# Kernel tuning notes

Hardware: AMD Instinct MI355X
Metric: run time of the kernel (lower is better)

The kernel has to match this reference:

```python
import jax, jax.numpy as jnp
import numpy as np
import math

INPUT_DIM = 1024
OUTPUT_DIM = 8192
M_BLOCKS = 8  # ceil(OUTPUT_DIM / INPUT_DIM)
SCALE = 1.0


def fwht(x):
    """Unnormalized fast Walsh-Hadamard transform over the last axis.
    Matches the torch recursive-cat implementation (Sylvester/natural order).
    """
    n = x.shape[-1]
    lead = x.shape[:-1]
    h = 1
    while h < n:
        y = x.reshape(lead + (n // (2 * h), 2, h))
        a = y[..., 0, :]
        b = y[..., 1, :]
        x = jnp.stack([a + b, a - b], axis=-2).reshape(lead + (n,))
        h *= 2
    return x


def setup_inputs() -> dict:
    key = jax.random.key(0)
    kx, kb, kg, ks, kp, ku = jax.random.split(key, 6)
    x = jax.random.normal(kx, (8, 1024, INPUT_DIM), dtype=jnp.float32)
    B = jax.random.normal(kb, (M_BLOCKS, INPUT_DIM), dtype=jnp.float32)
    G = jax.random.normal(kg, (M_BLOCKS, INPUT_DIM), dtype=jnp.float32)
    S = jax.random.uniform(ks, (M_BLOCKS, INPUT_DIM), dtype=jnp.float32)
    P = jax.random.randint(kp, (M_BLOCKS, INPUT_DIM), 0, INPUT_DIM, dtype=jnp.int64)
    u_rand = jax.random.uniform(ku, (OUTPUT_DIM,), dtype=jnp.float32)
    return {"x": x, "B": B, "G": G, "S": S, "P": P, "u_rand": u_rand}


def reference(x, B, G, S, P, u_rand):
    d = INPUT_DIM
    # flatten all leading dims into rows: (R, 1, d)
    xr = x.reshape(-1, 1, d)
    Bx = xr * B                                   # (R, m, d)
    HBx = fwht(Bx)                                # (R, m, d)
    idx = jnp.broadcast_to(P[None], HBx.shape)    # per-block permutation gather
    PHBx = jnp.take_along_axis(HBx, idx, axis=-1)
    GPHBx = PHBx * G
    HGPHBx = fwht(GPHBx)
    SHGPHBx = HGPHBx * S
    norm_factor = 1.0 / (SCALE * math.sqrt(d))
    Vx = norm_factor * SHGPHBx.reshape(SHGPHBx.shape[0], -1)  # (R, m*d)
    result = Vx[:, :OUTPUT_DIM]
    # phi nonlinearity: cos(x + 2*pi*U) * sqrt(2/output_dim)
    phase = (2.0 * jnp.pi) * u_rand
    result = jnp.cos(result + phase) * math.sqrt(2.0 / OUTPUT_DIM)
    return result
```

## Files before the change

### kernel.cpp

```cpp
#include <hip/hip_runtime.h>
#include <math.h>


typedef unsigned uint2_ev __attribute__((ext_vector_type(2)));
typedef float    f32x4    __attribute__((ext_vector_type(4)));

template <int CTRL>
__device__ __forceinline__ float dpp_f(float x) {
    return __int_as_float(
        __builtin_amdgcn_mov_dpp(__float_as_int(x), CTRL, 0xF, 0xF, true));
}

#define DPP_XOR1 0xB1
#define DPP_XOR2 0x4E
#define DPP_XOR3 0x1B
#define DPP_HMIR 0x141
#define DPP_ROR8 0x128

__device__ __forceinline__ void pl16_pair(float& e0, float& e1) {
    uint2_ev r = __builtin_amdgcn_permlane16_swap(
        __float_as_uint(e0), __float_as_uint(e1), false, false);
    float s = __uint_as_float(r.x) + __uint_as_float(r.y);
    float d = __uint_as_float(r.x) - __uint_as_float(r.y);
    uint2_ev q = __builtin_amdgcn_permlane16_swap(
        __float_as_uint(s), __float_as_uint(d), false, false);
    e0 = __uint_as_float(q.x);
    e1 = __uint_as_float(q.y);
}

__device__ __forceinline__ void pl32_pair(float& e0, float& e1) {
    uint2_ev r = __builtin_amdgcn_permlane32_swap(
        __float_as_uint(e0), __float_as_uint(e1), false, false);
    float s = __uint_as_float(r.x) + __uint_as_float(r.y);
    float d = __uint_as_float(r.x) - __uint_as_float(r.y);
    uint2_ev q = __builtin_amdgcn_permlane32_swap(
        __float_as_uint(s), __float_as_uint(d), false, false);
    e0 = __uint_as_float(q.x);
    e1 = __uint_as_float(q.y);
}

__device__ __forceinline__ void fwht_full(float v[16], float sg0, float sg1,
                                          float sg2, float sg3) {
#pragma unroll
    for (int h = 1; h < 16; h <<= 1) {
#pragma unroll
        for (int k = 0; k < 16; ++k) {
            if (!(k & h)) {
                float a = v[k], b = v[k ^ h];
                v[k] = a + b;
                v[k ^ h] = a - b;
            }
        }
    }
#pragma unroll
    for (int k = 0; k < 16; ++k) v[k] = fmaf(v[k], sg0, dpp_f<DPP_XOR1>(v[k]));
#pragma unroll
    for (int k = 0; k < 16; ++k) v[k] = fmaf(v[k], sg1, dpp_f<DPP_XOR2>(v[k]));
#pragma unroll
    for (int k = 0; k < 16; ++k)
        v[k] = fmaf(v[k], sg2, dpp_f<DPP_XOR3>(dpp_f<DPP_HMIR>(v[k])));
#pragma unroll
    for (int k = 0; k < 16; ++k) v[k] = fmaf(v[k], sg3, dpp_f<DPP_ROR8>(v[k]));
#pragma unroll
    for (int p = 0; p < 8; ++p) pl16_pair(v[2 * p], v[2 * p + 1]);
#pragma unroll
    for (int p = 0; p < 8; ++p) pl32_pair(v[2 * p], v[2 * p + 1]);
}

__global__ __launch_bounds__(256) void fastfood_kernel(
    const float* __restrict__ x, const float* __restrict__ B,
    const float* __restrict__ G, const float* __restrict__ S,
    const int* __restrict__ P, const float* __restrict__ u_rand,
    float* __restrict__ out)
{
    __shared__ float lds[4 * 1088];
    const int lane = threadIdx.x & 63;
    const int wv   = threadIdx.x >> 6;
    const int gw   = blockIdx.x * 4 + wv;
    const int row  = gw >> 3;
    const int mo   = (gw & 7) << 10;

    const float sg0 = (lane & 1) ? -1.f : 1.f;
    const float sg1 = (lane & 2) ? -1.f : 1.f;
    const float sg2 = (lane & 4) ? -1.f : 1.f;
    const float sg3 = (lane & 8) ? -1.f : 1.f;

    float* wlds = lds + wv * 1088;
    float4* w4 = (float4*)(wlds + 16 * lane + 4 * (lane >> 2));

    const float c_arg = 0.03125f * 0.15915494309189535f;
    const float c_amp = 0.015625f;

    float v[16];

    {
        const float4* x4 = (const float4*)(x + (size_t)row * 1024 + 16 * lane);
        const float4* B4 = (const float4*)(B + mo + 16 * lane);
#pragma unroll
        for (int j = 0; j < 4; ++j) {
            float4 xt = x4[j];
            float4 bt = B4[j];
            v[4 * j + 0] = xt.x * bt.x;
            v[4 * j + 1] = xt.y * bt.y;
            v[4 * j + 2] = xt.z * bt.z;
            v[4 * j + 3] = xt.w * bt.w;
        }
    }

    fwht_full(v, sg0, sg1, sg2, sg3);

    const int4*   P4 = (const int4*)(P + mo);
    const float4* G4 = (const float4*)(G + mo);
    int4   pj[4];
    float4 gj[4];
#pragma unroll
    for (int j = 0; j < 4; ++j) {
        pj[j] = P4[64 * j + lane];
        gj[j] = G4[64 * j + lane];
    }

#pragma unroll
    for (int j = 0; j < 4; ++j)
        w4[j] = make_float4(v[4 * j + 0], v[4 * j + 1],
                            v[4 * j + 2], v[4 * j + 3]);

#pragma unroll
    for (int j = 0; j < 4; ++j) {
        int4 p = pj[j];
        float4 g = gj[j];
        v[4 * j + 0] = wlds[p.x + ((p.x >> 6) << 2)] * g.x;
        v[4 * j + 1] = wlds[p.y + ((p.y >> 6) << 2)] * g.y;
        v[4 * j + 2] = wlds[p.z + ((p.z >> 6) << 2)] * g.z;
        v[4 * j + 3] = wlds[p.w + ((p.w >> 6) << 2)] * g.w;
    }

    float4 sv[4], uv[4];
    {
        const float4* S4 = (const float4*)(S + mo);
        const float4* U4 = (const float4*)(u_rand + mo);
#pragma unroll
        for (int b = 0; b < 4; ++b) {
            int idx = b * 64 + lane;
            sv[b] = S4[idx];
            uv[b] = U4[idx];
        }
    }

    fwht_full(v, sg0, sg1, sg2, sg3);

    {
        f32x4* o4 = (f32x4*)(out + (size_t)row * 8192 + mo);
#pragma unroll
        for (int b = 0; b < 4; ++b) {
            int idx = b * 64 + lane;
            f32x4 rr;
            rr.x = __builtin_amdgcn_cosf(__builtin_amdgcn_fractf(
                       fmaf(v[4 * b + 0] * sv[b].x, c_arg, uv[b].x))) * c_amp;
            rr.y = __builtin_amdgcn_cosf(__builtin_amdgcn_fractf(
                       fmaf(v[4 * b + 1] * sv[b].y, c_arg, uv[b].y))) * c_amp;
            rr.z = __builtin_amdgcn_cosf(__builtin_amdgcn_fractf(
                       fmaf(v[4 * b + 2] * sv[b].z, c_arg, uv[b].z))) * c_amp;
            rr.w = __builtin_amdgcn_cosf(__builtin_amdgcn_fractf(
                       fmaf(v[4 * b + 3] * sv[b].w, c_arg, uv[b].w))) * c_amp;
            __builtin_nontemporal_store(rr, &o4[idx]);
        }
    }
}

extern "C" void kernel_launch(void* const* d_in, const int* in_sizes, int n_in,
                              void* d_out, int out_size, void* d_ws, size_t ws_size,
                              hipStream_t stream) {
    const float* x = (const float*)d_in[0];
    const float* B = (const float*)d_in[1];
    const float* G = (const float*)d_in[2];
    const float* S = (const float*)d_in[3];
    const int*   P = (const int*)d_in[4];
    const float* u = (const float*)d_in[5];
    float* out = (float*)d_out;

    dim3 grid(16384), block(256);
    hipLaunchKernelGGL(fastfood_kernel, grid, block, 0, stream,
                       x, B, G, S, P, u, out);
}
```

Before: 342.1 us.

## Process all eight blocks per wave with loop, reusing x row in registers

Each wave now handles one full row and loops over the eight output blocks instead of one wave per (row, block). The x row is loaded once with nontemporal loads and kept in registers, and the next block's B vector is prefetched a block ahead. Output stores become regular stores instead of nontemporal. The grid shrinks eightfold, which cuts x reloads but reduces parallelism and serializes per-wave work.

```diff
diff --git a/kernel.cpp b/kernel.cpp
--- a/kernel.cpp
+++ b/kernel.cpp
@@ -76,9 +76,7 @@
     __shared__ float lds[4 * 1088];
     const int lane = threadIdx.x & 63;
     const int wv   = threadIdx.x >> 6;
-    const int gw   = blockIdx.x * 4 + wv;
-    const int row  = gw >> 3;
-    const int mo   = (gw & 7) << 10;
+    const int row  = blockIdx.x * 4 + wv;
 
     const float sg0 = (lane & 1) ? -1.f : 1.f;
     const float sg1 = (lane & 2) ? -1.f : 1.f;
@@ -91,78 +89,103 @@
     const float c_arg = 0.03125f * 0.15915494309189535f;
     const float c_amp = 0.015625f;
 
-    float v[16];
-
+    float xv[16];
     {
-        const float4* x4 = (const float4*)(x + (size_t)row * 1024 + 16 * lane);
-        const float4* B4 = (const float4*)(B + mo + 16 * lane);
+        const f32x4* x4 = (const f32x4*)(x + (size_t)row * 1024 + 16 * lane);
 #pragma unroll
         for (int j = 0; j < 4; ++j) {
-            float4 xt = x4[j];
-            float4 bt = B4[j];
-            v[4 * j + 0] = xt.x * bt.x;
-            v[4 * j + 1] = xt.y * bt.y;
-            v[4 * j + 2] = xt.z * bt.z;
-            v[4 * j + 3] = xt.w * bt.w;
-        }
-    }
-
-    fwht_full(v, sg0, sg1, sg2, sg3);
-
-    const int4*   P4 = (const int4*)(P + mo);
-    const float4* G4 = (const float4*)(G + mo);
-    int4   pj[4];
-    float4 gj[4];
-#pragma unroll
-    for (int j = 0; j < 4; ++j) {
-        pj[j] = P4[64 * j + lane];
-        gj[j] = G4[64 * j + lane];
-    }
-
-#pragma unroll
-    for (int j = 0; j < 4; ++j)
-        w4[j] = make_float4(v[4 * j + 0], v[4 * j + 1],
-                            v[4 * j + 2], v[4 * j + 3]);
-
-#pragma unroll
-    for (int j = 0; j < 4; ++j) {
-        int4 p = pj[j];
-        float4 g = gj[j];
-        v[4 * j + 0] = wlds[p.x + ((p.x >> 6) << 2)] * g.x;
-        v[4 * j + 1] = wlds[p.y + ((p.y >> 6) << 2)] * g.y;
-        v[4 * j + 2] = wlds[p.z + ((p.z >> 6) << 2)] * g.z;
-        v[4 * j + 3] = wlds[p.w + ((p.w >> 6) << 2)] * g.w;
-    }
-
-    float4 sv[4], uv[4];
+            f32x4 t = __builtin_nontemporal_load(&x4[j]);
+            xv[4 * j + 0] = t.x; xv[4 * j + 1] = t.y;
+            xv[4 * j + 2] = t.z; xv[4 * j + 3] = t.w;
+        }
+    }
+
+    float4 Bn0, Bn1, Bn2, Bn3;
     {
-        const float4* S4 = (const float4*)(S + mo);
-        const float4* U4 = (const float4*)(u_rand + mo);
-#pragma unroll
-        for (int b = 0; b < 4; ++b) {
-            int idx = b * 64 + lane;
-            sv[b] = S4[idx];
-            uv[b] = U4[idx];
-        }
-    }
-
-    fwht_full(v, sg0, sg1, sg2, sg3);
-
-    {
-        f32x4* o4 = (f32x4*)(out + (size_t)row * 8192 + mo);
-#pragma unroll
-        for (int b = 0; b < 4; ++b) {
-            int idx = b * 64 + lane;
-            f32x4 rr;
-            rr.x = __builtin_amdgcn_cosf(__builtin_amdgcn_fractf(
-                       fmaf(v[4 * b + 0] * sv[b].x, c_arg, uv[b].x))) * c_amp;
-            rr.y = __builtin_amdgcn_cosf(__builtin_amdgcn_fractf(
-                       fmaf(v[4 * b + 1] * sv[b].y, c_arg, uv[b].y))) * c_amp;
-            rr.z = __builtin_amdgcn_cosf(__builtin_amdgcn_fractf(
-                       fmaf(v[4 * b + 2] * sv[b].z, c_arg, uv[b].z))) * c_amp;
-            rr.w = __builtin_amdgcn_cosf(__builtin_amdgcn_fractf(
-                       fmaf(v[4 * b + 3] * sv[b].w, c_arg, uv[b].w))) * c_amp;
-            __builtin_nontemporal_store(rr, &o4[idx]);
+        const float4* B4 = (const float4*)(B + 16 * lane);
+        Bn0 = B4[0]; Bn1 = B4[1]; Bn2 = B4[2]; Bn3 = B4[3];
+    }
+
+#pragma unroll 1
+    for (int m = 0; m < 8; ++m) {
+        const int mo = m << 10;
+
+        float4 Bc0 = Bn0, Bc1 = Bn1, Bc2 = Bn2, Bc3 = Bn3;
+        {
+            const float4* Bq =
+                (const float4*)(B + (m < 7 ? mo + 1024 : mo) + 16 * lane);
+            Bn0 = Bq[0]; Bn1 = Bq[1]; Bn2 = Bq[2]; Bn3 = Bq[3];
+        }
+
+        float v[16];
+        v[0]  = xv[0]  * Bc0.x; v[1]  = xv[1]  * Bc0.y;
+        v[2]  = xv[2]  * Bc0.z; v[3]  = xv[3]  * Bc0.w;
+        v[4]  = xv[4]  * Bc1.x; v[5]  = xv[5]  * Bc1.y;
+        v[6]  = xv[6]  * Bc1.z; v[7]  = xv[7]  * Bc1.w;
+        v[8]  = xv[8]  * Bc2.x; v[9]  = xv[9]  * Bc2.y;
+        v[10] = xv[10] * Bc2.z; v[11] = xv[11] * Bc2.w;
+        v[12] = xv[12] * Bc3.x; v[13] = xv[13] * Bc3.y;
+        v[14] = xv[14] * Bc3.z; v[15] = xv[15] * Bc3.w;
+
+        int4   pj[4];
+        float4 gj[4];
+        {
+            const int4*   P4 = (const int4*)(P + mo);
+            const float4* G4 = (const float4*)(G + mo);
+#pragma unroll
+            for (int j = 0; j < 4; ++j) {
+                pj[j] = P4[64 * j + lane];
+                gj[j] = G4[64 * j + lane];
+            }
+        }
+
+        fwht_full(v, sg0, sg1, sg2, sg3);
+
+#pragma unroll
+        for (int j = 0; j < 4; ++j)
+            w4[j] = make_float4(v[4 * j + 0], v[4 * j + 1],
+                                v[4 * j + 2], v[4 * j + 3]);
+
+        float4 sv[4], uv[4];
+        {
+            const float4* S4 = (const float4*)(S + mo);
+            const float4* U4 = (const float4*)(u_rand + mo);
+#pragma unroll
+            for (int b = 0; b < 4; ++b) {
+                int idx = b * 64 + lane;
+                sv[b] = S4[idx];
+                uv[b] = U4[idx];
+            }
+        }
+
+#pragma unroll
+        for (int j = 0; j < 4; ++j) {
+            int4 p = pj[j];
+            float4 g = gj[j];
+            v[4 * j + 0] = wlds[p.x + ((p.x >> 6) << 2)] * g.x;
+            v[4 * j + 1] = wlds[p.y + ((p.y >> 6) << 2)] * g.y;
+            v[4 * j + 2] = wlds[p.z + ((p.z >> 6) << 2)] * g.z;
+            v[4 * j + 3] = wlds[p.w + ((p.w >> 6) << 2)] * g.w;
+        }
+
+        fwht_full(v, sg0, sg1, sg2, sg3);
+
+        {
+            float4* o4 = (float4*)(out + (size_t)row * 8192 + mo);
+#pragma unroll
+            for (int b = 0; b < 4; ++b) {
+                int idx = b * 64 + lane;
+                float4 rr;
+                rr.x = __builtin_amdgcn_cosf(__builtin_amdgcn_fractf(
+                           fmaf(v[4 * b + 0] * sv[b].x, c_arg, uv[b].x))) * c_amp;
+                rr.y = __builtin_amdgcn_cosf(__builtin_amdgcn_fractf(
+                           fmaf(v[4 * b + 1] * sv[b].y, c_arg, uv[b].y))) * c_amp;
+                rr.z = __builtin_amdgcn_cosf(__builtin_amdgcn_fractf(
+                           fmaf(v[4 * b + 2] * sv[b].z, c_arg, uv[b].z))) * c_amp;
+                rr.w = __builtin_amdgcn_cosf(__builtin_amdgcn_fractf(
+                           fmaf(v[4 * b + 3] * sv[b].w, c_arg, uv[b].w))) * c_amp;
+                o4[idx] = rr;
+            }
         }
     }
 }
@@ -178,7 +201,7 @@
     const float* u = (const float*)d_in[5];
     float* out = (float*)d_out;
 
-    dim3 grid(16384), block(256);
+    dim3 grid(2048), block(256);
     hipLaunchKernelGGL(fastfood_kernel, grid, block, 0, stream,
                        x, B, G, S, P, u, out);
 }
```

After: 347.1 us. No clear change (+1.5%).
